# Optimization experiments

Hardware: AMD Instinct MI355X
Metric: run time of the kernel (lower is better)

The kernel has to match this reference:

```python
import jax, jax.numpy as jnp
import numpy as np

B, T, U = 4, 256, 64
D_ENC, D_DEC, V = 512, 512, 1024
IN_F = D_ENC + D_DEC  # 1024


def setup_inputs() -> dict:
    key = jax.random.key(0)
    ks = jax.random.split(key, 10)
    enc = jax.random.normal(ks[0], (B, T, D_ENC), dtype=jnp.float32)
    dec = jax.random.normal(ks[1], (B, U, D_DEC), dtype=jnp.float32)
    # ragged lengths in [len/2, len]; force max to be attained so padded
    # shape equals the torch packed output shape (MaxPad == (T, U)).
    enc_lens = jax.random.randint(ks[2], (B,), T // 2, T + 1, dtype=jnp.int32).at[0].set(T)
    dec_lens = jax.random.randint(ks[3], (B,), U // 2, U + 1, dtype=jnp.int32).at[0].set(U)
    s_e = 1.0 / np.sqrt(D_ENC)
    s_d = 1.0 / np.sqrt(D_DEC)
    s_f = 1.0 / np.sqrt(IN_F)
    W_enc = jax.random.uniform(ks[4], (D_ENC, IN_F), jnp.float32, -s_e, s_e)
    b_enc = jax.random.uniform(ks[5], (IN_F,), jnp.float32, -s_e, s_e)
    W_dec = jax.random.uniform(ks[6], (D_DEC, IN_F), jnp.float32, -s_d, s_d)
    b_dec = jax.random.uniform(ks[7], (IN_F,), jnp.float32, -s_d, s_d)
    W_fc = jax.random.uniform(ks[8], (IN_F, V), jnp.float32, -s_f, s_f)
    b_fc = jax.random.uniform(ks[9], (V,), jnp.float32, -s_f, s_f)
    return dict(enc=enc, dec=dec, W_enc=W_enc, b_enc=b_enc, W_dec=W_dec,
                b_dec=b_dec, W_fc=W_fc, b_fc=b_fc,
                enc_lens=enc_lens, dec_lens=dec_lens)


def reference(enc, dec, W_enc, b_enc, W_dec, b_dec, W_fc, b_fc, enc_lens, dec_lens):
    # per-frame / per-label projections: [B,T,IN_F], [B,U,IN_F]
    pe = jnp.einsum('btd,df->btf', enc, W_enc) + b_enc
    pd = jnp.einsum('bud,df->buf', dec, W_dec) + b_dec
    # broadcast-add joint grid: [B,T,U,IN_F]
    h = pe[:, :, None, :] + pd[:, None, :, :]
    logits = jnp.einsum('btuf,fv->btuv', jnp.tanh(h), W_fc) + b_fc
    logp = jax.nn.log_softmax(logits, axis=-1)
    # zero out cells beyond (enc_len_b, dec_len_b), matching F.pad(value=0.)
    t_ok = jnp.arange(T)[None, :] < enc_lens[:, None]          # [B,T]
    u_ok = jnp.arange(U)[None, :] < dec_lens[:, None]          # [B,U]
    mask = (t_ok[:, :, None] & u_ok[:, None, :])[..., None]    # [B,T,U,1]
    return jnp.where(mask, logp, 0.0)
```

## Files before the change

### kernel.cpp

```cpp
#include <hip/hip_runtime.h>
#include <hip/hip_bf16.h>


#define TT 256
#define UU 64
#define VV 1024
#define FF 1024
#define DK 512

typedef __bf16 bf16x8 __attribute__((ext_vector_type(8)));
typedef float  f32x16 __attribute__((ext_vector_type(16)));
typedef int    i32x4v __attribute__((ext_vector_type(4)));
typedef int    i32x16 __attribute__((ext_vector_type(16)));

__device__ __forceinline__ float fast_tanh(float x) {
  float ax = __builtin_fabsf(x);
  float e  = __expf(-2.0f * ax);
  float r  = (1.0f - e) * __builtin_amdgcn_rcpf(1.0f + e);
  return __builtin_copysignf(r, x);
}

__global__ __launch_bounds__(256)
void prep_w(const float* __restrict__ Wenc, const float* __restrict__ Wdec,
            const float* __restrict__ Wfc,
            __bf16* __restrict__ Pen, __bf16* __restrict__ Pde,
            signed char* __restrict__ Pq, float* __restrict__ sc)
{
  int bi = blockIdx.x;
  int tid = threadIdx.x;
  if (bi < 512) {
    const float* W = (bi < 256) ? Wenc : Wdec;
    __bf16* P = (bi < 256) ? Pen : Pde;
    int base = (bi < 256) ? bi : bi - 256;
    int idx = base * 256 + tid;
    int k8 = idx >> 10, v = idx & 1023;
    bf16x8 o;
#pragma unroll
    for (int j = 0; j < 8; ++j) o[j] = (__bf16)W[(k8 * 8 + j) * 1024 + v];
    *(bf16x8*)(P + (size_t)idx * 8) = o;
    return;
  }
  __shared__ float mx[4][64];
  __shared__ float smax[64];
  int blk = bi - 512;
  int p = tid >> 6;
  int c = tid & 63;
  int v = blk * 64 + c;
  float m = 0.f;
#pragma unroll 8
  for (int k = p * 256; k < p * 256 + 256; ++k)
    m = fmaxf(m, __builtin_fabsf(Wfc[k * 1024 + v]));
  mx[p][c] = m;
  __syncthreads();
  float mm = fmaxf(fmaxf(mx[0][c], mx[1][c]), fmaxf(mx[2][c], mx[3][c]));
  if (p == 0) { smax[c] = mm; sc[v] = (mm > 0.f) ? mm / 127.f : 1.f; }
  __syncthreads();
  float si = (smax[c] > 0.f) ? 127.f / smax[c] : 0.f;
  for (int k16 = p * 16; k16 < p * 16 + 16; ++k16) {
    unsigned int w[4];
#pragma unroll
    for (int g = 0; g < 4; ++g) {
      unsigned int a = 0;
#pragma unroll
      for (int j = 0; j < 4; ++j) {
        float x = Wfc[(k16 * 16 + g * 4 + j) * 1024 + v];
        int q = (int)rintf(x * si);
        q = q > 127 ? 127 : (q < -127 ? -127 : q);
        a |= (unsigned int)(q & 255) << (8 * j);
      }
      w[g] = a;
    }
    *(uint4*)(Pq + ((size_t)k16 * 1024 + v) * 16) = make_uint4(w[0], w[1], w[2], w[3]);
  }
}

__global__ __launch_bounds__(256)
void proj_mfma(const float* __restrict__ enc, const float* __restrict__ dec,
               const __bf16* __restrict__ Pen, const __bf16* __restrict__ Pde,
               const float* __restrict__ be, const float* __restrict__ bd,
               float* __restrict__ pe, float* __restrict__ pd)
{
  constexpr int BK = 128;
  __shared__ __align__(16) char As[2][64 * BK * 2];
  const int tid = threadIdx.x;
  const int lane = tid & 63;
  const int wid  = tid >> 6;
  const int l31  = lane & 31;
  const int lhi  = lane >> 5;

  int bi = blockIdx.x;
  const float* X; const __bf16* PW; const float* bias; float* P; int rt, ct;
  if (bi < 64) { X = enc; PW = Pen; bias = be; P = pe; rt = bi >> 2; ct = bi & 3; }
  else { int bj = bi - 64; X = dec; PW = Pde; bias = bd; P = pd; rt = bj >> 2; ct = bj & 3; }
  const int r0 = rt * 64;

  auto fillA = [&](int buf, int kc) {
#pragma unroll
    for (int i = 0; i < 4; ++i) {
      int tau = i * 256 + tid;
      int r = tau >> 4, g = tau & 15;
      int k = kc * BK + g * 8;
      const float4* x4 = (const float4*)(X + (r0 + r) * DK + k);
      float4 a0 = x4[0], a1 = x4[1];
      float xv[8] = {a0.x, a0.y, a0.z, a0.w, a1.x, a1.y, a1.z, a1.w};
      bf16x8 p;
#pragma unroll
      for (int q = 0; q < 8; ++q) p[q] = (__bf16)xv[q];
      *(bf16x8*)(&As[buf][r * (BK * 2) + ((g * 16) ^ ((r & 7) << 4))]) = p;
    }
  };

  f32x16 acc[2][2];
#pragma unroll
  for (int mi = 0; mi < 2; ++mi)
#pragma unroll
    for (int ni = 0; ni < 2; ++ni)
#pragma unroll
      for (int q = 0; q < 16; ++q) acc[mi][ni][q] = 0.f;

  fillA(0, 0);
  __syncthreads();
  const int colBase = ct * 256 + wid * 64 + l31;
  for (int kc = 0; kc < DK / BK; ++kc) {
    if (kc + 1 < DK / BK) fillA((kc + 1) & 1, kc + 1);
    const char* Ab = As[kc & 1];
#pragma unroll 2
    for (int ks = 0; ks < BK / 16; ++ks) {
      int k8 = (kc * 8 + ks) * 2 + lhi;
      bf16x8 bfr[2];
#pragma unroll
      for (int ni = 0; ni < 2; ++ni)
        bfr[ni] = *(const bf16x8*)(PW + ((size_t)k8 * VV + colBase + ni * 32) * 8);
      bf16x8 afr[2];
#pragma unroll
      for (int mi = 0; mi < 2; ++mi) {
        int ra = mi * 32 + l31;
        int kb = ks * 32 + lhi * 16;
        afr[mi] = *(const bf16x8*)(&Ab[ra * (BK * 2) + (kb ^ ((ra & 7) << 4))]);
      }
#pragma unroll
      for (int mi = 0; mi < 2; ++mi)
#pragma unroll
        for (int ni = 0; ni < 2; ++ni)
          acc[mi][ni] = __builtin_amdgcn_mfma_f32_32x32x16_bf16(afr[mi], bfr[ni], acc[mi][ni], 0, 0, 0);
    }
    __syncthreads();
  }
  float bv[2];
#pragma unroll
  for (int ni = 0; ni < 2; ++ni) bv[ni] = bias[colBase + ni * 32];
#pragma unroll
  for (int mi = 0; mi < 2; ++mi)
#pragma unroll
    for (int j = 0; j < 16; ++j) {
      int row = r0 + mi * 32 + (j & 3) + 8 * (j >> 2) + 4 * lhi;
#pragma unroll
      for (int ni = 0; ni < 2; ++ni)
        P[row * VV + colBase + ni * 32] = acc[mi][ni][j] + bv[ni];
    }
}

__global__ __launch_bounds__(512, 2)
void joint_main(const float* __restrict__ pe, const float* __restrict__ pd,
                const signed char* __restrict__ Pq, const float* __restrict__ sc,
                const float* __restrict__ bfc,
                const int* __restrict__ elens, const int* __restrict__ dlens,
                float* __restrict__ out)
{
  __shared__ __align__(16) unsigned char Ab[65536];
  __shared__ float pr[8][64];
  __shared__ float lseS[64];

  const int blk = blockIdx.x;
  const int b = blk >> 8;
  const int t = blk & 255;
  const int tid = threadIdx.x;
  const int elen = elens[b], dlen = dlens[b];
  float* outBase = out + (size_t)blk * (UU * VV);

  if (t >= elen) {
    float4 z = {0.f, 0.f, 0.f, 0.f};
#pragma unroll 4
    for (int i = tid; i < UU * VV / 4; i += 512) ((float4*)outBase)[i] = z;
    return;
  }

  const int lane = tid & 63;
  const int wid  = tid >> 6;
  const int l31  = lane & 31;
  const int lhi  = lane >> 5;
  const int colLane = wid * 128 + l31;

  const float* peRow  = pe + (size_t)blk * FF;
  const float* pdBase = pd + (size_t)b * UU * FF;

  {
    const int row = tid >> 3;
    const float* pdRow = pdBase + (size_t)row * FF;
#pragma unroll
    for (int j = 0; j < 8; ++j) {
      int k16 = ((tid & 7) << 3) + j;
      const float4* e4 = (const float4*)(peRow + k16 * 16);
      const float4* d4 = (const float4*)(pdRow + k16 * 16);
      unsigned int w[4];
#pragma unroll
      for (int g = 0; g < 4; ++g) {
        float4 e = e4[g], d = d4[g];
        float h0 = e.x + d.x, h1 = e.y + d.y, h2 = e.z + d.z, h3 = e.w + d.w;
        unsigned int a = 0;
        a |= (unsigned int)(((int)rintf(fast_tanh(h0) * 127.f)) & 255);
        a |= (unsigned int)(((int)rintf(fast_tanh(h1) * 127.f)) & 255) << 8;
        a |= (unsigned int)(((int)rintf(fast_tanh(h2) * 127.f)) & 255) << 16;
        a |= (unsigned int)(((int)rintf(fast_tanh(h3) * 127.f)) & 255) << 24;
        w[g] = a;
      }
      *(uint4*)(&Ab[((k16 << 6) + row) << 4]) = make_uint4(w[0], w[1], w[2], w[3]);
    }
  }
  __syncthreads();

  i32x4v bq[4][4];
  auto loadB = [&](int kc) {
    const signed char* gp = Pq + (size_t)kc * 32768;
#pragma unroll
    for (int ni = 0; ni < 4; ++ni)
      bq[kc & 3][ni] = *(const i32x4v*)(gp +
          ((size_t)((lhi << 10) + colLane + (ni << 5)) << 4));
  };

  i32x16 acc[2][4];
#pragma unroll
  for (int mi = 0; mi < 2; ++mi)
#pragma unroll
    for (int ni = 0; ni < 4; ++ni)
#pragma unroll
      for (int q = 0; q < 16; ++q) acc[mi][ni][q] = 0;

  loadB(0); loadB(1); loadB(2); loadB(3);

#pragma unroll
  for (int kc = 0; kc < 32; ++kc) {
    i32x4v afr[2];
#pragma unroll
    for (int mi = 0; mi < 2; ++mi)
      afr[mi] = *(const i32x4v*)(&Ab[((((kc << 1) + lhi) << 6) + mi * 32 + l31) << 4]);
#pragma unroll
    for (int mi = 0; mi < 2; ++mi)
#pragma unroll
      for (int ni = 0; ni < 4; ++ni)
        acc[mi][ni] = __builtin_amdgcn_mfma_i32_32x32x32_i8(afr[mi], bq[kc & 3][ni],
                                                            acc[mi][ni], 0, 0, 0);
    if (kc + 4 < 32) loadB(kc + 4);
  }

  float bias[4], scl[4];
#pragma unroll
  for (int ni = 0; ni < 4; ++ni) {
    bias[ni] = bfc[colLane + ni * 32];
    scl[ni]  = sc[colLane + ni * 32] * (1.f / 127.f);
  }

  float rsum[2][16];
#pragma unroll
  for (int mi = 0; mi < 2; ++mi)
#pragma unroll
    for (int j = 0; j < 16; ++j) {
      float su = 0.f;
#pragma unroll
      for (int ni = 0; ni < 4; ++ni) {
        float v = (float)acc[mi][ni][j] * scl[ni] + bias[ni];
        acc[mi][ni][j] = __float_as_int(v);
        su += __expf(v);
      }
      rsum[mi][j] = su;
    }
#pragma unroll
  for (int st = 1; st < 32; st <<= 1) {
#pragma unroll
    for (int mi = 0; mi < 2; ++mi)
#pragma unroll
      for (int j = 0; j < 16; ++j)
        rsum[mi][j] += __shfl_xor(rsum[mi][j], st, 64);
  }
#pragma unroll
  for (int mi = 0; mi < 2; ++mi)
#pragma unroll
    for (int j = 0; j < 16; ++j)
      if (l31 == j) {
        int row = mi * 32 + (j & 3) + 8 * (j >> 2) + 4 * lhi;
        pr[wid][row] = rsum[mi][j];
      }
  __syncthreads();
  if (tid < 64) {
    float su = 0.f;
#pragma unroll
    for (int w = 0; w < 8; ++w) su += pr[w][tid];
    lseS[tid] = __logf(su);
  }
  __syncthreads();

#pragma unroll
  for (int mi = 0; mi < 2; ++mi)
#pragma unroll
    for (int j = 0; j < 16; ++j) {
      int row = mi * 32 + (j & 3) + 8 * (j >> 2) + 4 * lhi;
      float l = lseS[row];
      bool valid = row < dlen;
#pragma unroll
      for (int ni = 0; ni < 4; ++ni) {
        float v = valid ? (__int_as_float(acc[mi][ni][j]) - l) : 0.0f;
        outBase[(size_t)row * VV + colLane + ni * 32] = v;
      }
    }
}

extern "C" void kernel_launch(void* const* d_in, const int* in_sizes, int n_in,
                              void* d_out, int out_size, void* d_ws, size_t ws_size,
                              hipStream_t stream)
{
  const float* enc  = (const float*)d_in[0];
  const float* dec  = (const float*)d_in[1];
  const float* Wenc = (const float*)d_in[2];
  const float* benc = (const float*)d_in[3];
  const float* Wdec = (const float*)d_in[4];
  const float* bdec = (const float*)d_in[5];
  const float* Wfc  = (const float*)d_in[6];
  const float* bfc  = (const float*)d_in[7];
  const int* elens  = (const int*)d_in[8];
  const int* dlens  = (const int*)d_in[9];
  float* out = (float*)d_out;

  float* pe = (float*)d_ws;
  float* pd = pe + 1024 * 1024;
  __bf16* Pen = (__bf16*)(pd + 256 * 1024);
  __bf16* Pde = Pen + 512 * 1024;
  signed char* Pq = (signed char*)(Pde + 512 * 1024);
  float* sc = (float*)(Pq + 1024 * 1024);

  prep_w<<<528, 256, 0, stream>>>(Wenc, Wdec, Wfc, Pen, Pde, Pq, sc);
  proj_mfma<<<80, 256, 0, stream>>>(enc, dec, Pen, Pde, benc, bdec, pe, pd);
  joint_main<<<1024, 512, 0, stream>>>(pe, pd, Pq, sc, bfc, elens, dlens, out);
}
```

Before: 240.7 us.

## Process two encoder frames per joint block to share weight-tile loads

The joint kernel now handles two consecutive t positions per block: 1024 threads, a 128-row A tile in LDS (128KB), and 16 waves arranged as 2 row groups by 8 column groups. Each int8 W_fc tile fetched from global memory now feeds twice as many MFMA rows, which roughly halves weight traffic per output. The cost is double the LDS per block, so only one block fits per CU. The launch bound of (1024, 4) may also tighten register allocation and cause spills. Masking now checks the per-row t against enc_len. The proj kernel change is a cosmetic rename of the LDS buffer reference.

Result: slower. 941.3 us (+291.0%).

```diff
diff --git a/kernel.cpp b/kernel.cpp
--- a/kernel.cpp
+++ b/kernel.cpp
@@ -136,7 +136,7 @@
       for (int mi = 0; mi < 2; ++mi) {
         int ra = mi * 32 + l31;
         int kb = ks * 32 + lhi * 16;
-        afr[mi] = *(const bf16x8*)(&Ab[ra * (BK * 2) + (kb ^ ((ra & 7) << 4))]);
+        afr[mi] = *(const bf16x8*)(&As[kc & 1][ra * (BK * 2) + (kb ^ ((ra & 7) << 4))]);
       }
 #pragma unroll
       for (int mi = 0; mi < 2; ++mi)
@@ -160,48 +160,50 @@
     }
 }
 
-__global__ __launch_bounds__(512, 2)
+__global__ __launch_bounds__(1024, 4)
 void joint_main(const float* __restrict__ pe, const float* __restrict__ pd,
                 const signed char* __restrict__ Pq, const float* __restrict__ sc,
                 const float* __restrict__ bfc,
                 const int* __restrict__ elens, const int* __restrict__ dlens,
                 float* __restrict__ out)
 {
-  __shared__ __align__(16) unsigned char Ab[65536];
-  __shared__ float pr[8][64];
-  __shared__ float lseS[64];
+  __shared__ __align__(16) unsigned char Ab[131072];
+  __shared__ float pr[8][128];
+  __shared__ float lseS[128];
 
   const int blk = blockIdx.x;
-  const int b = blk >> 8;
-  const int t = blk & 255;
+  const int b = blk >> 7;
+  const int t0 = (blk & 127) << 1;
   const int tid = threadIdx.x;
   const int elen = elens[b], dlen = dlens[b];
-  float* outBase = out + (size_t)blk * (UU * VV);
-
-  if (t >= elen) {
+  float* outBase = out + (size_t)(b * TT + t0) * (UU * VV);
+
+  if (t0 >= elen) {
     float4 z = {0.f, 0.f, 0.f, 0.f};
 #pragma unroll 4
-    for (int i = tid; i < UU * VV / 4; i += 512) ((float4*)outBase)[i] = z;
+    for (int i = tid; i < 2 * UU * VV / 4; i += 1024) ((float4*)outBase)[i] = z;
     return;
   }
 
   const int lane = tid & 63;
   const int wid  = tid >> 6;
+  const int wr   = wid >> 3;
+  const int wc   = wid & 7;
   const int l31  = lane & 31;
   const int lhi  = lane >> 5;
-  const int colLane = wid * 128 + l31;
-
-  const float* peRow  = pe + (size_t)blk * FF;
-  const float* pdBase = pd + (size_t)b * UU * FF;
+  const int colLane = wc * 128 + l31;
+
+  const float* peB = pe + (size_t)(b * TT + t0) * FF;
+  const float* pdB = pd + (size_t)b * UU * FF;
 
   {
-    const int row = tid >> 3;
-    const float* pdRow = pdBase + (size_t)row * FF;
 #pragma unroll
     for (int j = 0; j < 8; ++j) {
-      int k16 = ((tid & 7) << 3) + j;
-      const float4* e4 = (const float4*)(peRow + k16 * 16);
-      const float4* d4 = (const float4*)(pdRow + k16 * 16);
+      int k16 = wid * 4 + (j & 3);
+      int row = lane + ((j >> 2) << 6);
+      int tl = row >> 6, u = row & 63;
+      const float4* e4 = (const float4*)(peB + tl * FF + k16 * 16);
+      const float4* d4 = (const float4*)(pdB + (size_t)u * FF + k16 * 16);
       unsigned int w[4];
 #pragma unroll
       for (int g = 0; g < 4; ++g) {
@@ -214,7 +216,7 @@
         a |= (unsigned int)(((int)rintf(fast_tanh(h3) * 127.f)) & 255) << 24;
         w[g] = a;
       }
-      *(uint4*)(&Ab[((k16 << 6) + row) << 4]) = make_uint4(w[0], w[1], w[2], w[3]);
+      *(uint4*)(&Ab[((k16 << 7) + row) << 4]) = make_uint4(w[0], w[1], w[2], w[3]);
     }
   }
   __syncthreads();
@@ -243,7 +245,7 @@
     i32x4v afr[2];
 #pragma unroll
     for (int mi = 0; mi < 2; ++mi)
-      afr[mi] = *(const i32x4v*)(&Ab[((((kc << 1) + lhi) << 6) + mi * 32 + l31) << 4]);
+      afr[mi] = *(const i32x4v*)(&Ab[((((kc << 1) + lhi) << 7) + wr * 64 + mi * 32 + l31) << 4]);
 #pragma unroll
     for (int mi = 0; mi < 2; ++mi)
 #pragma unroll
@@ -287,11 +289,11 @@
 #pragma unroll
     for (int j = 0; j < 16; ++j)
       if (l31 == j) {
-        int row = mi * 32 + (j & 3) + 8 * (j >> 2) + 4 * lhi;
-        pr[wid][row] = rsum[mi][j];
-      }
-  __syncthreads();
-  if (tid < 64) {
+        int row = wr * 64 + mi * 32 + (j & 3) + 8 * (j >> 2) + 4 * lhi;
+        pr[wc][row] = rsum[mi][j];
+      }
+  __syncthreads();
+  if (tid < 128) {
     float su = 0.f;
 #pragma unroll
     for (int w = 0; w < 8; ++w) su += pr[w][tid];
@@ -303,9 +305,9 @@
   for (int mi = 0; mi < 2; ++mi)
 #pragma unroll
     for (int j = 0; j < 16; ++j) {
-      int row = mi * 32 + (j & 3) + 8 * (j >> 2) + 4 * lhi;
+      int row = wr * 64 + mi * 32 + (j & 3) + 8 * (j >> 2) + 4 * lhi;
       float l = lseS[row];
-      bool valid = row < dlen;
+      bool valid = ((t0 + (row >> 6)) < elen) && ((row & 63) < dlen);
 #pragma unroll
       for (int ni = 0; ni < 4; ++ni) {
         float v = valid ? (__int_as_float(acc[mi][ni][j]) - l) : 0.0f;
@@ -339,5 +341,5 @@
 
   prep_w<<<528, 256, 0, stream>>>(Wenc, Wdec, Wfc, Pen, Pde, Pq, sc);
   proj_mfma<<<80, 256, 0, stream>>>(enc, dec, Pen, Pde, benc, bdec, pe, pd);
-  joint_main<<<1024, 512, 0, stream>>>(pe, pd, Pq, sc, bfc, elens, dlens, out);
-}
+  joint_main<<<512, 1024, 0, stream>>>(pe, pd, Pq, sc, bfc, elens, dlens, out);
+}
```

## Split joint kernel into activation build, tiled int8 GEMM, and log-softmax passes

Applied to the files above, without the earlier changes.

Replaces the fused per-(b,t) joint kernel with three kernels. The first materializes the quantized tanh activations to a global buffer. The second is a 128x128 tiled int8 MFMA GEMM that double-buffers A and B through LDS with global_load_lds and writes raw logits. The third is a separate row-wise log-softmax and masking pass that rereads and rewrites the 256MB output. The aim is better weight reuse and better tiling than the per-row fused design, at the cost of extra global traffic: the intermediate activation buffer plus a full second read/write of the output.

Result: slower. 347.3 us (+44.3%).

```diff
diff --git a/kernel.cpp b/kernel.cpp
--- a/kernel.cpp
+++ b/kernel.cpp
@@ -160,158 +160,174 @@
     }
 }
 
-__global__ __launch_bounds__(512, 2)
-void joint_main(const float* __restrict__ pe, const float* __restrict__ pd,
-                const signed char* __restrict__ Pq, const float* __restrict__ sc,
-                const float* __restrict__ bfc,
-                const int* __restrict__ elens, const int* __restrict__ dlens,
-                float* __restrict__ out)
-{
-  __shared__ __align__(16) unsigned char Ab[65536];
-  __shared__ float pr[8][64];
-  __shared__ float lseS[64];
-
-  const int blk = blockIdx.x;
-  const int b = blk >> 8;
-  const int t = blk & 255;
+__global__ __launch_bounds__(256)
+void abuild(const float* __restrict__ pe, const float* __restrict__ pd,
+            signed char* __restrict__ Af)
+{
+  const int bt = blockIdx.x;
+  const int b  = bt >> 8;
   const int tid = threadIdx.x;
-  const int elen = elens[b], dlen = dlens[b];
-  float* outBase = out + (size_t)blk * (UU * VV);
-
-  if (t >= elen) {
-    float4 z = {0.f, 0.f, 0.f, 0.f};
-#pragma unroll 4
-    for (int i = tid; i < UU * VV / 4; i += 512) ((float4*)outBase)[i] = z;
-    return;
-  }
-
+  const int wid = tid >> 6;
+  const int lane = tid & 63;
+  const int row = bt * 64 + lane;
+  const float* peRow = pe + (size_t)bt * FF;
+  const float* pdRow = pd + (size_t)(b * 64 + lane) * FF;
+
+#pragma unroll
+  for (int j = 0; j < 16; ++j) {
+    int k16 = wid * 16 + j;
+    const float4* e4 = (const float4*)(peRow + k16 * 16);
+    const float4* d4 = (const float4*)(pdRow + k16 * 16);
+    unsigned int w[4];
+#pragma unroll
+    for (int g = 0; g < 4; ++g) {
+      float4 e = e4[g], d = d4[g];
+      float h0 = e.x + d.x, h1 = e.y + d.y, h2 = e.z + d.z, h3 = e.w + d.w;
+      unsigned int a = 0;
+      a |= (unsigned int)(((int)rintf(fast_tanh(h0) * 127.f)) & 255);
+      a |= (unsigned int)(((int)rintf(fast_tanh(h1) * 127.f)) & 255) << 8;
+      a |= (unsigned int)(((int)rintf(fast_tanh(h2) * 127.f)) & 255) << 16;
+      a |= (unsigned int)(((int)rintf(fast_tanh(h3) * 127.f)) & 255) << 24;
+      w[g] = a;
+    }
+    *(uint4*)(Af + (((size_t)k16 << 16) + row) * 16) = make_uint4(w[0], w[1], w[2], w[3]);
+  }
+}
+
+__global__ __launch_bounds__(256)
+void gemm128(const signed char* __restrict__ Af, const signed char* __restrict__ Pq,
+             const float* __restrict__ sc, const float* __restrict__ bfc,
+             const int* __restrict__ elens,
+             float* __restrict__ out)
+{
+  __shared__ __align__(16) unsigned char As[2][8192];
+  __shared__ __align__(16) unsigned char Bs[2][8192];
+
+  const int bid  = blockIdx.x;
+  const int bidn = bid & 7;
+  const int bidm = bid >> 3;
+  const int R0 = bidm * 128;
+  const int C0 = bidn * 128;
+
+  const int bt0 = R0 >> 6;
+  const int b   = bt0 >> 8;
+  const int t0  = bt0 & 255;
+  if (t0 >= elens[b]) return;
+
+  const int tid = threadIdx.x;
   const int lane = tid & 63;
   const int wid  = tid >> 6;
+  const int wr   = wid >> 1;
+  const int wc   = wid & 1;
   const int l31  = lane & 31;
   const int lhi  = lane >> 5;
-  const int colLane = wid * 128 + l31;
-
-  const float* peRow  = pe + (size_t)blk * FF;
-  const float* pdBase = pd + (size_t)b * UU * FF;
-
-  {
-    const int row = tid >> 3;
-    const float* pdRow = pdBase + (size_t)row * FF;
-#pragma unroll
-    for (int j = 0; j < 8; ++j) {
-      int k16 = ((tid & 7) << 3) + j;
-      const float4* e4 = (const float4*)(peRow + k16 * 16);
-      const float4* d4 = (const float4*)(pdRow + k16 * 16);
-      unsigned int w[4];
-#pragma unroll
-      for (int g = 0; g < 4; ++g) {
-        float4 e = e4[g], d = d4[g];
-        float h0 = e.x + d.x, h1 = e.y + d.y, h2 = e.z + d.z, h3 = e.w + d.w;
-        unsigned int a = 0;
-        a |= (unsigned int)(((int)rintf(fast_tanh(h0) * 127.f)) & 255);
-        a |= (unsigned int)(((int)rintf(fast_tanh(h1) * 127.f)) & 255) << 8;
-        a |= (unsigned int)(((int)rintf(fast_tanh(h2) * 127.f)) & 255) << 16;
-        a |= (unsigned int)(((int)rintf(fast_tanh(h3) * 127.f)) & 255) << 24;
-        w[g] = a;
+
+  auto fill = [&](int buf, int kc) {
+#pragma unroll
+    for (int half = 0; half < 2; ++half) {
+      __builtin_amdgcn_global_load_lds(
+        (const __attribute__((address_space(1))) void*)
+          (Af + ((((size_t)(kc * 4 + wid)) << 16) + R0 + half * 64 + lane) * 16),
+        (__attribute__((address_space(3))) void*)(&As[buf][(wid * 128 + half * 64) * 16]),
+        16, 0, 0);
+      __builtin_amdgcn_global_load_lds(
+        (const __attribute__((address_space(1))) void*)
+          (Pq + ((((size_t)(kc * 4 + wid)) << 10) + C0 + half * 64 + lane) * 16),
+        (__attribute__((address_space(3))) void*)(&Bs[buf][(wid * 128 + half * 64) * 16]),
+        16, 0, 0);
+    }
+  };
+
+  i32x16 acc[2][2];
+#pragma unroll
+  for (int mi = 0; mi < 2; ++mi)
+#pragma unroll
+    for (int ni = 0; ni < 2; ++ni)
+#pragma unroll
+      for (int q = 0; q < 16; ++q) acc[mi][ni][q] = 0;
+
+  fill(0, 0);
+  __syncthreads();
+
+  for (int kc = 0; kc < 16; ++kc) {
+    if (kc + 1 < 16) fill((kc + 1) & 1, kc + 1);
+    const unsigned char* Ap = As[kc & 1];
+    const unsigned char* Bp = Bs[kc & 1];
+#pragma unroll
+    for (int s = 0; s < 2; ++s) {
+      const int g = s * 2 + lhi;
+      i32x4v afr[2], bfr[2];
+#pragma unroll
+      for (int mi = 0; mi < 2; ++mi)
+        afr[mi] = *(const i32x4v*)(Ap + ((g << 7) + wr * 64 + mi * 32 + l31) * 16);
+#pragma unroll
+      for (int ni = 0; ni < 2; ++ni)
+        bfr[ni] = *(const i32x4v*)(Bp + ((g << 7) + wc * 64 + ni * 32 + l31) * 16);
+#pragma unroll
+      for (int mi = 0; mi < 2; ++mi)
+#pragma unroll
+        for (int ni = 0; ni < 2; ++ni)
+          acc[mi][ni] = __builtin_amdgcn_mfma_i32_32x32x32_i8(afr[mi], bfr[ni],
+                                                              acc[mi][ni], 0, 0, 0);
+    }
+    __syncthreads();
+  }
+
+  float scl[2], bias[2];
+#pragma unroll
+  for (int ni = 0; ni < 2; ++ni) {
+    int col = C0 + wc * 64 + ni * 32 + l31;
+    scl[ni]  = sc[col] * (1.f / 127.f);
+    bias[ni] = bfc[col];
+  }
+#pragma unroll
+  for (int mi = 0; mi < 2; ++mi)
+#pragma unroll
+    for (int j = 0; j < 16; ++j) {
+      int row = R0 + wr * 64 + mi * 32 + (j & 3) + 8 * (j >> 2) + 4 * lhi;
+#pragma unroll
+      for (int ni = 0; ni < 2; ++ni) {
+        int col = C0 + wc * 64 + ni * 32 + l31;
+        out[((size_t)row << 10) + col] = (float)acc[mi][ni][j] * scl[ni] + bias[ni];
       }
-      *(uint4*)(&Ab[((k16 << 6) + row) << 4]) = make_uint4(w[0], w[1], w[2], w[3]);
-    }
-  }
-  __syncthreads();
-
-  i32x4v bq[4][4];
-  auto loadB = [&](int kc) {
-    const signed char* gp = Pq + (size_t)kc * 32768;
-#pragma unroll
-    for (int ni = 0; ni < 4; ++ni)
-      bq[kc & 3][ni] = *(const i32x4v*)(gp +
-          ((size_t)((lhi << 10) + colLane + (ni << 5)) << 4));
-  };
-
-  i32x16 acc[2][4];
-#pragma unroll
-  for (int mi = 0; mi < 2; ++mi)
-#pragma unroll
-    for (int ni = 0; ni < 4; ++ni)
-#pragma unroll
-      for (int q = 0; q < 16; ++q) acc[mi][ni][q] = 0;
-
-  loadB(0); loadB(1); loadB(2); loadB(3);
-
-#pragma unroll
-  for (int kc = 0; kc < 32; ++kc) {
-    i32x4v afr[2];
-#pragma unroll
-    for (int mi = 0; mi < 2; ++mi)
-      afr[mi] = *(const i32x4v*)(&Ab[((((kc << 1) + lhi) << 6) + mi * 32 + l31) << 4]);
-#pragma unroll
-    for (int mi = 0; mi < 2; ++mi)
-#pragma unroll
-      for (int ni = 0; ni < 4; ++ni)
-        acc[mi][ni] = __builtin_amdgcn_mfma_i32_32x32x32_i8(afr[mi], bq[kc & 3][ni],
-                                                            acc[mi][ni], 0, 0, 0);
-    if (kc + 4 < 32) loadB(kc + 4);
-  }
-
-  float bias[4], scl[4];
-#pragma unroll
-  for (int ni = 0; ni < 4; ++ni) {
-    bias[ni] = bfc[colLane + ni * 32];
-    scl[ni]  = sc[colLane + ni * 32] * (1.f / 127.f);
-  }
-
-  float rsum[2][16];
-#pragma unroll
-  for (int mi = 0; mi < 2; ++mi)
-#pragma unroll
-    for (int j = 0; j < 16; ++j) {
-      float su = 0.f;
-#pragma unroll
-      for (int ni = 0; ni < 4; ++ni) {
-        float v = (float)acc[mi][ni][j] * scl[ni] + bias[ni];
-        acc[mi][ni][j] = __float_as_int(v);
-        su += __expf(v);
-      }
-      rsum[mi][j] = su;
-    }
-#pragma unroll
-  for (int st = 1; st < 32; st <<= 1) {
-#pragma unroll
-    for (int mi = 0; mi < 2; ++mi)
-#pragma unroll
-      for (int j = 0; j < 16; ++j)
-        rsum[mi][j] += __shfl_xor(rsum[mi][j], st, 64);
-  }
-#pragma unroll
-  for (int mi = 0; mi < 2; ++mi)
-#pragma unroll
-    for (int j = 0; j < 16; ++j)
-      if (l31 == j) {
-        int row = mi * 32 + (j & 3) + 8 * (j >> 2) + 4 * lhi;
-        pr[wid][row] = rsum[mi][j];
-      }
-  __syncthreads();
-  if (tid < 64) {
-    float su = 0.f;
-#pragma unroll
-    for (int w = 0; w < 8; ++w) su += pr[w][tid];
-    lseS[tid] = __logf(su);
-  }
-  __syncthreads();
-
-#pragma unroll
-  for (int mi = 0; mi < 2; ++mi)
-#pragma unroll
-    for (int j = 0; j < 16; ++j) {
-      int row = mi * 32 + (j & 3) + 8 * (j >> 2) + 4 * lhi;
-      float l = lseS[row];
-      bool valid = row < dlen;
-#pragma unroll
-      for (int ni = 0; ni < 4; ++ni) {
-        float v = valid ? (__int_as_float(acc[mi][ni][j]) - l) : 0.0f;
-        outBase[(size_t)row * VV + colLane + ni * 32] = v;
-      }
-    }
+    }
+}
+
+__global__ __launch_bounds__(256)
+void lsm(float* __restrict__ out,
+         const int* __restrict__ elens, const int* __restrict__ dlens)
+{
+  const int tid = threadIdx.x;
+  const int wid = tid >> 6;
+  const int lane = tid & 63;
+  const int r = blockIdx.x * 4 + wid;
+  const int b = r >> 14;
+  const int t = (r >> 6) & 255;
+  const int u = r & 63;
+  float* rowp = out + ((size_t)r << 10) + lane * 16;
+
+  const bool masked = (t >= elens[b]) || (u >= dlens[b]);
+  if (masked) {
+    float4 z = {0.f, 0.f, 0.f, 0.f};
+#pragma unroll
+    for (int g = 0; g < 4; ++g) ((float4*)rowp)[g] = z;
+    return;
+  }
+  float4 v[4];
+  float s = 0.f;
+#pragma unroll
+  for (int g = 0; g < 4; ++g) {
+    v[g] = ((const float4*)rowp)[g];
+    s += __expf(v[g].x) + __expf(v[g].y) + __expf(v[g].z) + __expf(v[g].w);
+  }
+#pragma unroll
+  for (int st = 1; st < 64; st <<= 1) s += __shfl_xor(s, st, 64);
+  const float lse = __logf(s);
+#pragma unroll
+  for (int g = 0; g < 4; ++g) {
+    v[g].x -= lse; v[g].y -= lse; v[g].z -= lse; v[g].w -= lse;
+    ((float4*)rowp)[g] = v[g];
+  }
 }
 
 extern "C" void kernel_launch(void* const* d_in, const int* in_sizes, int n_in,
@@ -336,8 +352,11 @@
   __bf16* Pde = Pen + 512 * 1024;
   signed char* Pq = (signed char*)(Pde + 512 * 1024);
   float* sc = (float*)(Pq + 1024 * 1024);
+  signed char* Af = (signed char*)(sc + 1024);
 
   prep_w<<<528, 256, 0, stream>>>(Wenc, Wdec, Wfc, Pen, Pde, Pq, sc);
   proj_mfma<<<80, 256, 0, stream>>>(enc, dec, Pen, Pde, benc, bdec, pe, pd);
-  joint_main<<<1024, 512, 0, stream>>>(pe, pd, Pq, sc, bfc, elens, dlens, out);
-}
+  abuild<<<1024, 256, 0, stream>>>(pe, pd, Af);
+  gemm128<<<4096, 256, 0, stream>>>(Af, Pq, sc, bfc, elens, out);
+  lsm<<<16384, 256, 0, stream>>>(out, elens, dlens);
+}
```
